# Optimization experiments

Measured on AMD Instinct MI355X. Metric: run time of the kernel, lower is better.

Reference implementation:

```python
import jax, jax.numpy as jnp
import numpy as np

WS = 8          # window_size
SHIFT = 4       # shift_size
NUM_HEADS = 8
DIM = 256
HIDDEN = 1024   # mlp_ratio * dim
EPS = 1e-5


def _rel_pos_index(ws):
    # static numpy computation of Swin relative position index, shape (ws*ws, ws*ws)
    coords = np.stack(np.meshgrid(np.arange(ws), np.arange(ws), indexing='ij')).reshape(2, -1)
    rel = coords[:, :, None] - coords[:, None, :]            # (2, N, N)
    rel = rel.transpose(1, 2, 0).astype(np.int64)            # (N, N, 2)
    rel[..., 0] += ws - 1
    rel[..., 1] += ws - 1
    rel[..., 0] *= 2 * ws - 1
    return rel.sum(-1)                                       # (N, N)

_REL_IDX = _rel_pos_index(WS)


def _layer_norm(x, g, b):
    m = jnp.mean(x, axis=-1, keepdims=True)
    v = jnp.mean(jnp.square(x - m), axis=-1, keepdims=True)
    return (x - m) * jax.lax.rsqrt(v + EPS) * g + b


def _window_partition(x, ws):
    B, H, W, C = x.shape
    x = x.reshape(B, H // ws, ws, W // ws, ws, C)
    return x.transpose(0, 1, 3, 2, 4, 5).reshape(-1, ws * ws, C)


def _window_reverse(win, ws, B, H, W):
    C = win.shape[-1]
    x = win.reshape(B, H // ws, W // ws, ws, ws, C)
    return x.transpose(0, 1, 3, 2, 4, 5).reshape(B, H, W, C)


def setup_inputs() -> dict:
    key = jax.random.key(0)
    ks = jax.random.split(key, 16)
    s = 0.02
    inp = {
        'x': jax.random.normal(ks[0], (8, 16384, 256), jnp.float32),
        'norm1_w': jnp.ones((DIM,), jnp.float32),
        'norm1_b': jnp.zeros((DIM,), jnp.float32),
        'qkv_w': jax.random.normal(ks[1], (3 * DIM, DIM), jnp.float32) * s,
        'qkv_b': jnp.zeros((3 * DIM,), jnp.float32),
        'rpb_table': jax.random.normal(ks[2], ((2 * WS - 1) * (2 * WS - 1), NUM_HEADS), jnp.float32) * s,
        'proj_w': jax.random.normal(ks[3], (DIM, DIM), jnp.float32) * s,
        'proj_b': jnp.zeros((DIM,), jnp.float32),
        'norm2_w': jnp.ones((DIM,), jnp.float32),
        'norm2_b': jnp.zeros((DIM,), jnp.float32),
        'fc1_w': jax.random.normal(ks[4], (HIDDEN, DIM), jnp.float32) * s,
        'fc1_b': jnp.zeros((HIDDEN,), jnp.float32),
        'fc2_w': jax.random.normal(ks[5], (DIM, HIDDEN), jnp.float32) * s,
        'fc2_b': jnp.zeros((DIM,), jnp.float32),
        'h': 128,
        'w': 128,
    }
    return inp


def reference(x, norm1_w, norm1_b, qkv_w, qkv_b, rpb_table, proj_w, proj_b,
              norm2_w, norm2_b, fc1_w, fc1_b, fc2_w, fc2_b, h, w):
    B, L, C = x.shape
    H, W = int(h), int(w)
    nh, hd = NUM_HEADS, C // NUM_HEADS
    scale = hd ** -0.5
    N = WS * WS

    shortcut = x
    xn = _layer_norm(x, norm1_w, norm1_b).reshape(B, H, W, C)
    # cyclic shift (SW-MSA)
    xs = jnp.roll(xn, shift=(-SHIFT, -SHIFT), axis=(1, 2))
    xw = _window_partition(xs, WS)                           # (B_, N, C)

    # window attention
    qkv = xw @ qkv_w.T + qkv_b                               # (B_, N, 3C)
    qkv = qkv.reshape(-1, N, 3, nh, hd).transpose(2, 0, 3, 1, 4)
    q, k, v = qkv[0], qkv[1], qkv[2]                         # (B_, nh, N, hd)
    attn = jnp.einsum('bhnd,bhmd->bhnm', q * scale, k)
    bias = rpb_table[_REL_IDX.reshape(-1)].reshape(N, N, nh).transpose(2, 0, 1)
    attn = jax.nn.softmax(attn + bias[None], axis=-1)
    out = jnp.einsum('bhnm,bhmd->bhnd', attn, v)
    out = out.transpose(0, 2, 1, 3).reshape(-1, N, C)
    out = out @ proj_w.T + proj_b

    # merge windows and reverse shift
    xs = _window_reverse(out, WS, B, H, W)
    xo = jnp.roll(xs, shift=(SHIFT, SHIFT), axis=(1, 2)).reshape(B, H * W, C)

    x = shortcut + xo
    # MLP with residual
    y = _layer_norm(x, norm2_w, norm2_b)
    y = jax.nn.gelu(y @ fc1_w.T + fc1_b, approximate=False)
    y = y @ fc2_w.T + fc2_b
    return x + y
```

## Files before the change

kernel.cpp:

```cpp
#include <hip/hip_runtime.h>

typedef __bf16 bf16_t;
typedef __bf16 bf16x4 __attribute__((ext_vector_type(4)));
typedef __bf16 bf16x8 __attribute__((ext_vector_type(8)));
typedef float f32x4 __attribute__((ext_vector_type(4)));

#define QKV_SEG 33554432L

#define GLDS(gp, lp)                                                                   \
  __builtin_amdgcn_global_load_lds((const __attribute__((address_space(1))) void*)(gp), \
                                   (__attribute__((address_space(3))) void*)(lp), 16, 0, 0)
#define BAR __builtin_amdgcn_s_barrier()
#define SCHED0 __builtin_amdgcn_sched_barrier(0)
#define MFMA __builtin_amdgcn_mfma_f32_16x16x32_bf16

__device__ inline float gelu_f(float u) {
  float c2 = 1.5957691216057308f * (u + 0.044715f * u * u * u);
  return u - u / (__expf(c2) + 1.0f);
}

__global__ __launch_bounds__(256) void cvt_kernel(const float* __restrict__ src,
                                                  bf16_t* __restrict__ dst) {
  int i = (blockIdx.x * 256 + threadIdx.x) * 4;
  float4 v = *(const float4*)(src + i);
  bf16x4 o;
  o[0] = (bf16_t)v.x; o[1] = (bf16_t)v.y; o[2] = (bf16_t)v.z; o[3] = (bf16_t)v.w;
  *(bf16x4*)(dst + i) = o;
}

__global__ __launch_bounds__(256) void ln_kernel(const float* __restrict__ src,
                                                 const float* __restrict__ gw,
                                                 const float* __restrict__ gb,
                                                 bf16_t* __restrict__ dst) {
  int lane = threadIdx.x & 63, wv = threadIdx.x >> 6;
  long m = (long)blockIdx.x * 4 + wv;
  long b_ = m >> 6; int tok = (int)(m & 63);
  int bb = (int)(b_ >> 8), win = (int)(b_ & 255);
  int wh = win >> 4, ww = win & 15;
  int ii = tok >> 3, jj = tok & 7;
  int hh = (wh * 8 + ii + 4) & 127, wp = (ww * 8 + jj + 4) & 127;
  long srow = ((long)bb << 14) + (hh << 7) + wp;

  float4 v = *(const float4*)(src + srow * 256 + lane * 4);
  float s = v.x + v.y + v.z + v.w;
  float s2 = v.x * v.x + v.y * v.y + v.z * v.z + v.w * v.w;
#pragma unroll
  for (int msk = 1; msk < 64; msk <<= 1) {
    s += __shfl_xor(s, msk);
    s2 += __shfl_xor(s2, msk);
  }
  float mean = s * (1.f / 256.f);
  float var = s2 * (1.f / 256.f) - mean * mean;
  float rs = rsqrtf(var + 1e-5f);
  float4 g4 = *(const float4*)(gw + lane * 4);
  float4 b4 = *(const float4*)(gb + lane * 4);
  bf16x4 o;
  o[0] = (bf16_t)((v.x - mean) * rs * g4.x + b4.x);
  o[1] = (bf16_t)((v.y - mean) * rs * g4.y + b4.y);
  o[2] = (bf16_t)((v.z - mean) * rs * g4.z + b4.z);
  o[3] = (bf16_t)((v.w - mean) * rs * g4.w + b4.w);
  *(bf16x4*)(dst + m * 256 + lane * 4) = o;
}

template <int EPI>
__global__ __launch_bounds__(256) void gemm_kernel(const bf16_t* __restrict__ A,
                                                   const bf16_t* __restrict__ Bw,
                                                   const float* __restrict__ bias, int K,
                                                   bf16_t* __restrict__ out_bf,
                                                   const float* resid) {
  __shared__ __align__(16) bf16_t As[2][8192];
  __shared__ __align__(16) bf16_t Bs[2][8192];
  int tid = threadIdx.x;
  int lane = tid & 63, wv = tid >> 6;
  int wm = wv >> 1, wn = wv & 1;

  int GX = gridDim.x, GY = gridDim.y;
  int flat = blockIdx.x + blockIdx.y * GX;
  int xcd = flat & 7, ii = flat >> 3;
  int iq = ii / GX;
  int by = xcd * (GY >> 3) + iq;
  int bx = ii - iq * GX;
  long m0 = (long)by * 128;
  int n0 = bx * 128;
  int lr = lane & 15, g = lane >> 4;

  int csw = (((lane & 7) ^ (lane >> 3)) << 3);
  const bf16_t* gA = A + (m0 + wv * 32 + (lane >> 3)) * K + csw;
  const bf16_t* gB = Bw + (long)(n0 + wv * 32 + (lane >> 3)) * K + csw;

  f32x4 acc[4][4] = {};

#define STAGE(buf, k0)                                                    \
  do {                                                                    \
    _Pragma("unroll") for (int s = 0; s < 4; ++s) {                       \
      GLDS(gA + (long)s * 8 * K + (k0), As[buf] + wv * 2048 + s * 512);   \
      GLDS(gB + (long)s * 8 * K + (k0), Bs[buf] + wv * 2048 + s * 512);   \
    }                                                                     \
  } while (0)

  int nt = K >> 6;
  STAGE(0, 0);
  for (int t = 0; t < nt; ++t) {
    int tb = t & 1;
    if (t + 1 < nt) {
      STAGE(tb ^ 1, (t + 1) << 6);
      asm volatile("s_waitcnt vmcnt(8)" ::: "memory");
    } else {
      asm volatile("s_waitcnt vmcnt(0)" ::: "memory");
    }
    BAR;
    SCHED0;
#pragma unroll
    for (int kk = 0; kk < 2; ++kk) {
      bf16x8 af[4], bfr[4];
#pragma unroll
      for (int mf = 0; mf < 4; ++mf)
        af[mf] = *(const bf16x8*)(As[tb] + (wm * 64 + mf * 16 + lr) * 64 +
                                  (((kk * 4 + g) ^ (lr & 7)) << 3));
#pragma unroll
      for (int nf = 0; nf < 4; ++nf)
        bfr[nf] = *(const bf16x8*)(Bs[tb] + (wn * 64 + nf * 16 + lr) * 64 +
                                   (((kk * 4 + g) ^ (lr & 7)) << 3));
#pragma unroll
      for (int mf = 0; mf < 4; ++mf)
#pragma unroll
        for (int nf = 0; nf < 4; ++nf)
          acc[mf][nf] = MFMA(af[mf], bfr[nf], acc[mf][nf], 0, 0, 0);
    }
    BAR;
  }
#undef STAGE

#pragma unroll
  for (int mf = 0; mf < 4; ++mf) {
#pragma unroll
    for (int nf = 0; nf < 4; ++nf) {
      long mb = m0 + wm * 64 + mf * 16 + 4 * g;
      int n = n0 + wn * 64 + nf * 16 + lr;
      float bn = bias[n];
      if (EPI == 0) {
        long b_ = mb >> 6;
        int tok = (int)(mb & 63);
        int which = n >> 8, rem = n & 255, head = rem >> 5, d = rem & 31;
        if (which == 2) {
          bf16x4 o;
#pragma unroll
          for (int r = 0; r < 4; ++r) o[r] = (bf16_t)(acc[mf][nf][r] + bn);
          *(bf16x4*)(out_bf + 2 * QKV_SEG + ((b_ * 8 + head) * 32 + d) * 64 + tok) = o;
        } else {
          long base = (long)which * QKV_SEG + ((b_ * 8 + head) * 64 + tok) * 32 + d;
#pragma unroll
          for (int r = 0; r < 4; ++r) out_bf[base + r * 32] = (bf16_t)(acc[mf][nf][r] + bn);
        }
      } else {
#pragma unroll
        for (int r = 0; r < 4; ++r) {
          long m = mb + r;
          long b_ = m >> 6; int tok = (int)(m & 63);
          int bb = (int)(b_ >> 8), win = (int)(b_ & 255);
          int wh = win >> 4, ww = win & 15;
          int jj0 = tok >> 3, jj = tok & 7;
          int hh = (wh * 8 + jj0 + 4) & 127, wp = (ww * 8 + jj + 4) & 127;
          long dst = (((long)bb << 14) + (hh << 7) + wp) * 256 + n;
          out_bf[dst] = (bf16_t)(acc[mf][nf][r] + bn + resid[dst]);
        }
      }
    }
  }
}

__global__ __launch_bounds__(512, 6) void mlp_kernel(const bf16_t* __restrict__ x1b,
                                                     float* __restrict__ out,
                                                     const float* __restrict__ gw,
                                                     const float* __restrict__ gb,
                                                     const bf16_t* __restrict__ w1,
                                                     const float* __restrict__ b1,
                                                     const bf16_t* __restrict__ w2,
                                                     const float* __restrict__ b2) {
  __shared__ __align__(16) bf16_t ys[64][264];
  __shared__ __align__(16) bf16_t hs[64][136];
  int tid = threadIdx.x, lane = tid & 63, wv = tid >> 6;
  long m0 = (long)blockIdx.x * 64;
  int lr = lane & 15, lk = (lane >> 4) * 8, g = lane >> 4;

  float4 g4 = *(const float4*)(gw + lane * 4);
  float4 b4 = *(const float4*)(gb + lane * 4);
#pragma unroll
  for (int i = 0; i < 8; ++i) {
    int r = wv * 8 + i;
    bf16x4 xv = *(const bf16x4*)(x1b + (m0 + r) * 256 + lane * 4);
    float v0 = (float)xv[0], v1 = (float)xv[1], v2 = (float)xv[2], v3 = (float)xv[3];
    float s = v0 + v1 + v2 + v3;
    float s2 = v0 * v0 + v1 * v1 + v2 * v2 + v3 * v3;
#pragma unroll
    for (int msk = 1; msk < 64; msk <<= 1) {
      s += __shfl_xor(s, msk);
      s2 += __shfl_xor(s2, msk);
    }
    float mean = s * (1.f / 256.f);
    float var = s2 * (1.f / 256.f) - mean * mean;
    float rs = rsqrtf(var + 1e-5f);
    bf16x4 o;
    o[0] = (bf16_t)((v0 - mean) * rs * g4.x + b4.x);
    o[1] = (bf16_t)((v1 - mean) * rs * g4.y + b4.y);
    o[2] = (bf16_t)((v2 - mean) * rs * g4.z + b4.z);
    o[3] = (bf16_t)((v3 - mean) * rs * g4.w + b4.w);
    *(bf16x4*)(&ys[r][lane * 4]) = o;
  }
  __syncthreads();

  f32x4 acc2[4][2] = {};

  for (int hc = 0; hc < 8; ++hc) {
    f32x4 acc1[4] = {};
#pragma unroll
    for (int half = 0; half < 2; ++half) {
      bf16x8 xf[4];
#pragma unroll
      for (int kb = 0; kb < 4; ++kb)
        xf[kb] = *(const bf16x8*)(w1 + (long)(hc * 128 + wv * 16 + lr) * 256 +
                                  (half * 4 + kb) * 32 + lk);
#pragma unroll
      for (int kb = 0; kb < 4; ++kb) {
        bf16x8 yf[4];
#pragma unroll
        for (int nt = 0; nt < 4; ++nt)
          yf[nt] = *(const bf16x8*)(&ys[nt * 16 + lr][(half * 4 + kb) * 32 + lk]);
#pragma unroll
        for (int nt = 0; nt < 4; ++nt) acc1[nt] = MFMA(xf[kb], yf[nt], acc1[nt], 0, 0, 0);
      }
    }
    {
      float4 bb = *(const float4*)(b1 + hc * 128 + wv * 16 + 4 * g);
#pragma unroll
      for (int nt = 0; nt < 4; ++nt) {
        bf16x4 o;
#pragma unroll
        for (int r = 0; r < 4; ++r) o[r] = (bf16_t)gelu_f(acc1[nt][r] + ((const float*)&bb)[r]);
        *(bf16x4*)(&hs[nt * 16 + lr][wv * 16 + 4 * g]) = o;
      }
    }
    __syncthreads();
#pragma unroll
    for (int half = 0; half < 2; ++half) {
      bf16x8 bw[2][2];
#pragma unroll
      for (int kb = 0; kb < 2; ++kb)
#pragma unroll
        for (int nf = 0; nf < 2; ++nf)
          bw[kb][nf] = *(const bf16x8*)(w2 + (long)(wv * 32 + nf * 16 + lr) * 1024 + hc * 128 +
                                        (half * 2 + kb) * 32 + lk);
#pragma unroll
      for (int kb = 0; kb < 2; ++kb) {
        bf16x8 ah[4];
#pragma unroll
        for (int mf = 0; mf < 4; ++mf)
          ah[mf] = *(const bf16x8*)(&hs[mf * 16 + lr][(half * 2 + kb) * 32 + lk]);
#pragma unroll
        for (int mf = 0; mf < 4; ++mf)
#pragma unroll
          for (int nf = 0; nf < 2; ++nf)
            acc2[mf][nf] = MFMA(ah[mf], bw[kb][nf], acc2[mf][nf], 0, 0, 0);
      }
    }
    __syncthreads();
  }

#pragma unroll
  for (int mf = 0; mf < 4; ++mf)
#pragma unroll
    for (int nf = 0; nf < 2; ++nf) {
      int n = wv * 32 + nf * 16 + lr;
      float bn = b2[n];
#pragma unroll
      for (int r = 0; r < 4; ++r) {
        long row = m0 + mf * 16 + 4 * g + r;
        out[row * 256 + n] = acc2[mf][nf][r] + bn + (float)x1b[row * 256 + n];
      }
    }
}

__global__ __launch_bounds__(256) void attn_kernel(const bf16_t* __restrict__ qkv,
                                                   const float* __restrict__ rpb,
                                                   bf16_t* __restrict__ attn_out) {
  __shared__ float rpb_s[1800];
  __shared__ bf16_t P[4][64][72];
  int tid = threadIdx.x, lane = tid & 63, wv = tid >> 6;
  long b_ = blockIdx.x;
  for (int i = tid; i < 1800; i += 256) rpb_s[i] = rpb[i];
  __syncthreads();
  const bf16_t* q = qkv;
  const bf16_t* k = qkv + QKV_SEG;
  const bf16_t* vt = qkv + 2 * QKV_SEG;
  int lr = lane & 15, lk = (lane >> 4) * 8, g = lane >> 4;
  const float scale = 0.17677669529663688f;

  for (int hh = 0; hh < 2; ++hh) {
    int head = wv * 2 + hh;
    long base = (b_ * 8 + head) * 2048;
    bf16x8 af[4], bfr[4];
#pragma unroll
    for (int mf = 0; mf < 4; ++mf)
      af[mf] = *(const bf16x8*)(q + base + (mf * 16 + lr) * 32 + lk);
#pragma unroll
    for (int nf = 0; nf < 4; ++nf)
      bfr[nf] = *(const bf16x8*)(k + base + (nf * 16 + lr) * 32 + lk);
    f32x4 S[4][4] = {};
#pragma unroll
    for (int mf = 0; mf < 4; ++mf)
#pragma unroll
      for (int nf = 0; nf < 4; ++nf)
        S[mf][nf] = MFMA(af[mf], bfr[nf], S[mf][nf], 0, 0, 0);
#pragma unroll
    for (int mf = 0; mf < 4; ++mf)
#pragma unroll
      for (int nf = 0; nf < 4; ++nf)
#pragma unroll
        for (int r = 0; r < 4; ++r) {
          int i = mf * 16 + 4 * g + r, j = nf * 16 + lr;
          int rel = ((i >> 3) - (j >> 3) + 7) * 15 + ((i & 7) - (j & 7) + 7);
          S[mf][nf][r] = S[mf][nf][r] * scale + rpb_s[rel * 8 + head];
        }
#pragma unroll
    for (int mf = 0; mf < 4; ++mf) {
#pragma unroll
      for (int r = 0; r < 4; ++r) {
        float mx = fmaxf(fmaxf(S[mf][0][r], S[mf][1][r]), fmaxf(S[mf][2][r], S[mf][3][r]));
#pragma unroll
        for (int msk = 1; msk < 16; msk <<= 1) mx = fmaxf(mx, __shfl_xor(mx, msk));
        float sm = 0.f;
#pragma unroll
        for (int nf = 0; nf < 4; ++nf) {
          float e = __expf(S[mf][nf][r] - mx);
          S[mf][nf][r] = e;
          sm += e;
        }
#pragma unroll
        for (int msk = 1; msk < 16; msk <<= 1) sm += __shfl_xor(sm, msk);
        float is = 1.f / sm;
        int i = mf * 16 + 4 * g + r;
#pragma unroll
        for (int nf = 0; nf < 4; ++nf) P[wv][i][nf * 16 + lr] = (bf16_t)(S[mf][nf][r] * is);
      }
    }
    f32x4 O[4][2] = {};
#pragma unroll
    for (int ks = 0; ks < 2; ++ks) {
      int j0 = ks * 32;
      bf16x8 pa[4], vb[2];
#pragma unroll
      for (int mf = 0; mf < 4; ++mf) pa[mf] = *(const bf16x8*)(&P[wv][mf * 16 + lr][j0 + lk]);
#pragma unroll
      for (int nf = 0; nf < 2; ++nf)
        vb[nf] = *(const bf16x8*)(vt + base + (nf * 16 + lr) * 64 + j0 + lk);
#pragma unroll
      for (int mf = 0; mf < 4; ++mf)
#pragma unroll
        for (int nf = 0; nf < 2; ++nf)
          O[mf][nf] = MFMA(pa[mf], vb[nf], O[mf][nf], 0, 0, 0);
    }
#pragma unroll
    for (int mf = 0; mf < 4; ++mf)
#pragma unroll
      for (int nf = 0; nf < 2; ++nf)
#pragma unroll
        for (int r = 0; r < 4; ++r) {
          int i = mf * 16 + 4 * g + r, d = nf * 16 + lr;
          attn_out[(b_ * 64 + i) * 256 + head * 32 + d] = (bf16_t)O[mf][nf][r];
        }
  }
}

extern "C" void kernel_launch(void* const* d_in, const int* in_sizes, int n_in,
                              void* d_out, int out_size, void* d_ws, size_t ws_size,
                              hipStream_t stream) {
  const float* x = (const float*)d_in[0];
  const float* n1w = (const float*)d_in[1];
  const float* n1b = (const float*)d_in[2];
  const float* qkv_w = (const float*)d_in[3];
  const float* qkv_b = (const float*)d_in[4];
  const float* rpb = (const float*)d_in[5];
  const float* proj_w = (const float*)d_in[6];
  const float* proj_b = (const float*)d_in[7];
  const float* n2w = (const float*)d_in[8];
  const float* n2b = (const float*)d_in[9];
  const float* fc1_w = (const float*)d_in[10];
  const float* fc1_b = (const float*)d_in[11];
  const float* fc2_w = (const float*)d_in[12];
  const float* fc2_b = (const float*)d_in[13];
  float* out = (float*)d_out;

  char* ws = (char*)d_ws;
  bf16_t* bufA = (bf16_t*)ws;
  bf16_t* x1b = (bf16_t*)(ws + 201326592L);
  bf16_t* bufB = (bf16_t*)(ws + 268435456L);
  bf16_t* wq = (bf16_t*)(ws + 335544320L);
  bf16_t* wp = wq + 196608;
  bf16_t* w1 = wp + 65536;
  bf16_t* w2 = w1 + 262144;

  cvt_kernel<<<192, 256, 0, stream>>>(qkv_w, wq);
  cvt_kernel<<<64, 256, 0, stream>>>(proj_w, wp);
  cvt_kernel<<<256, 256, 0, stream>>>(fc1_w, w1);
  cvt_kernel<<<256, 256, 0, stream>>>(fc2_w, w2);

  ln_kernel<<<32768, 256, 0, stream>>>(x, n1w, n1b, bufB);
  gemm_kernel<0><<<dim3(6, 1024), 256, 0, stream>>>(bufB, wq, qkv_b, 256, bufA, nullptr);
  attn_kernel<<<2048, 256, 0, stream>>>(bufA, rpb, bufB);
  gemm_kernel<1><<<dim3(2, 1024), 256, 0, stream>>>(bufB, wp, proj_b, 256, x1b, x);
  mlp_kernel<<<2048, 512, 0, stream>>>(x1b, out, n2w, n2b, w1, fc1_b, w2, fc2_b);
}
```

Baseline: 602.4 us.

## Fuse output projection and residual into window attention kernel

```diff
diff --git a/kernel.cpp b/kernel.cpp
--- a/kernel.cpp
+++ b/kernel.cpp
@@ -62,12 +62,10 @@
   *(bf16x4*)(dst + m * 256 + lane * 4) = o;
 }
 
-template <int EPI>
 __global__ __launch_bounds__(256) void gemm_kernel(const bf16_t* __restrict__ A,
                                                    const bf16_t* __restrict__ Bw,
                                                    const float* __restrict__ bias, int K,
-                                                   bf16_t* __restrict__ out_bf,
-                                                   const float* resid) {
+                                                   bf16_t* __restrict__ out_bf) {
   __shared__ __align__(16) bf16_t As[2][8192];
   __shared__ __align__(16) bf16_t Bs[2][8192];
   int tid = threadIdx.x;
@@ -138,34 +136,160 @@
       long mb = m0 + wm * 64 + mf * 16 + 4 * g;
       int n = n0 + wn * 64 + nf * 16 + lr;
       float bn = bias[n];
-      if (EPI == 0) {
-        long b_ = mb >> 6;
-        int tok = (int)(mb & 63);
-        int which = n >> 8, rem = n & 255, head = rem >> 5, d = rem & 31;
-        if (which == 2) {
-          bf16x4 o;
-#pragma unroll
-          for (int r = 0; r < 4; ++r) o[r] = (bf16_t)(acc[mf][nf][r] + bn);
-          *(bf16x4*)(out_bf + 2 * QKV_SEG + ((b_ * 8 + head) * 32 + d) * 64 + tok) = o;
-        } else {
-          long base = (long)which * QKV_SEG + ((b_ * 8 + head) * 64 + tok) * 32 + d;
-#pragma unroll
-          for (int r = 0; r < 4; ++r) out_bf[base + r * 32] = (bf16_t)(acc[mf][nf][r] + bn);
+      long b_ = mb >> 6;
+      int tok = (int)(mb & 63);
+      int which = n >> 8, rem = n & 255, head = rem >> 5, d = rem & 31;
+      if (which == 2) {
+        bf16x4 o;
+#pragma unroll
+        for (int r = 0; r < 4; ++r) o[r] = (bf16_t)(acc[mf][nf][r] + bn);
+        *(bf16x4*)(out_bf + 2 * QKV_SEG + ((b_ * 8 + head) * 32 + d) * 64 + tok) = o;
+      } else {
+        long base = (long)which * QKV_SEG + ((b_ * 8 + head) * 64 + tok) * 32 + d;
+#pragma unroll
+        for (int r = 0; r < 4; ++r) out_bf[base + r * 32] = (bf16_t)(acc[mf][nf][r] + bn);
+      }
+    }
+  }
+}
+
+__global__ __launch_bounds__(256) void attn2_kernel(const bf16_t* __restrict__ qkv,
+                                                    const float* __restrict__ rpb,
+                                                    const bf16_t* __restrict__ wp,
+                                                    const float* __restrict__ proj_b,
+                                                    const float* __restrict__ x,
+                                                    bf16_t* __restrict__ x1b) {
+  __shared__ float rpb_s[1800];
+  __shared__ bf16_t P[4][64][72];
+  __shared__ bf16_t ao[64][264];
+  int tid = threadIdx.x, lane = tid & 63, wv = tid >> 6;
+  long b_ = blockIdx.x;
+  for (int i = tid; i < 1800; i += 256) rpb_s[i] = rpb[i];
+  __syncthreads();
+  const bf16_t* q = qkv;
+  const bf16_t* k = qkv + QKV_SEG;
+  const bf16_t* vt = qkv + 2 * QKV_SEG;
+  int lr = lane & 15, lk = (lane >> 4) * 8, g = lane >> 4;
+  const float scale = 0.17677669529663688f;
+
+  for (int hh = 0; hh < 2; ++hh) {
+    int head = wv * 2 + hh;
+    long base = (b_ * 8 + head) * 2048;
+    bf16x8 af[4], bfr[4];
+#pragma unroll
+    for (int mf = 0; mf < 4; ++mf)
+      af[mf] = *(const bf16x8*)(q + base + (mf * 16 + lr) * 32 + lk);
+#pragma unroll
+    for (int nf = 0; nf < 4; ++nf)
+      bfr[nf] = *(const bf16x8*)(k + base + (nf * 16 + lr) * 32 + lk);
+    f32x4 S[4][4] = {};
+#pragma unroll
+    for (int mf = 0; mf < 4; ++mf)
+#pragma unroll
+      for (int nf = 0; nf < 4; ++nf)
+        S[mf][nf] = MFMA(af[mf], bfr[nf], S[mf][nf], 0, 0, 0);
+#pragma unroll
+    for (int mf = 0; mf < 4; ++mf)
+#pragma unroll
+      for (int nf = 0; nf < 4; ++nf)
+#pragma unroll
+        for (int r = 0; r < 4; ++r) {
+          int i = mf * 16 + 4 * g + r, j = nf * 16 + lr;
+          int rel = ((i >> 3) - (j >> 3) + 7) * 15 + ((i & 7) - (j & 7) + 7);
+          S[mf][nf][r] = S[mf][nf][r] * scale + rpb_s[rel * 8 + head];
         }
-      } else {
+#pragma unroll
+    for (int mf = 0; mf < 4; ++mf) {
+#pragma unroll
+      for (int r = 0; r < 4; ++r) {
+        float mx = fmaxf(fmaxf(S[mf][0][r], S[mf][1][r]), fmaxf(S[mf][2][r], S[mf][3][r]));
+#pragma unroll
+        for (int msk = 1; msk < 16; msk <<= 1) mx = fmaxf(mx, __shfl_xor(mx, msk));
+        float sm = 0.f;
+#pragma unroll
+        for (int nf = 0; nf < 4; ++nf) {
+          float e = __expf(S[mf][nf][r] - mx);
+          S[mf][nf][r] = e;
+          sm += e;
+        }
+#pragma unroll
+        for (int msk = 1; msk < 16; msk <<= 1) sm += __shfl_xor(sm, msk);
+        float is = 1.f / sm;
+        int i = mf * 16 + 4 * g + r;
+#pragma unroll
+        for (int nf = 0; nf < 4; ++nf) P[wv][i][nf * 16 + lr] = (bf16_t)(S[mf][nf][r] * is);
+      }
+    }
+    f32x4 O[4][2] = {};
+#pragma unroll
+    for (int ks = 0; ks < 2; ++ks) {
+      int j0 = ks * 32;
+      bf16x8 pa[4], vb[2];
+#pragma unroll
+      for (int mf = 0; mf < 4; ++mf) pa[mf] = *(const bf16x8*)(&P[wv][mf * 16 + lr][j0 + lk]);
+#pragma unroll
+      for (int nf = 0; nf < 2; ++nf)
+        vb[nf] = *(const bf16x8*)(vt + base + (nf * 16 + lr) * 64 + j0 + lk);
+#pragma unroll
+      for (int mf = 0; mf < 4; ++mf)
+#pragma unroll
+        for (int nf = 0; nf < 2; ++nf)
+          O[mf][nf] = MFMA(pa[mf], vb[nf], O[mf][nf], 0, 0, 0);
+    }
+#pragma unroll
+    for (int mf = 0; mf < 4; ++mf)
+#pragma unroll
+      for (int nf = 0; nf < 2; ++nf)
 #pragma unroll
         for (int r = 0; r < 4; ++r) {
-          long m = mb + r;
-          long b_ = m >> 6; int tok = (int)(m & 63);
-          int bb = (int)(b_ >> 8), win = (int)(b_ & 255);
-          int wh = win >> 4, ww = win & 15;
-          int jj0 = tok >> 3, jj = tok & 7;
-          int hh = (wh * 8 + jj0 + 4) & 127, wp = (ww * 8 + jj + 4) & 127;
-          long dst = (((long)bb << 14) + (hh << 7) + wp) * 256 + n;
-          out_bf[dst] = (bf16_t)(acc[mf][nf][r] + bn + resid[dst]);
+          int i = mf * 16 + 4 * g + r, d = nf * 16 + lr;
+          ao[i][head * 32 + d] = (bf16_t)O[mf][nf][r];
         }
-      }
-    }
+  }
+  __syncthreads();
+
+  f32x4 pacc[4][4] = {};
+#pragma unroll
+  for (int half = 0; half < 4; ++half) {
+    bf16x8 bw[2][4];
+#pragma unroll
+    for (int kb = 0; kb < 2; ++kb)
+#pragma unroll
+      for (int nf = 0; nf < 4; ++nf)
+        bw[kb][nf] = *(const bf16x8*)(wp + (long)(wv * 64 + nf * 16 + lr) * 256 +
+                                      (half * 2 + kb) * 32 + lk);
+#pragma unroll
+    for (int kb = 0; kb < 2; ++kb) {
+      bf16x8 paf[4];
+#pragma unroll
+      for (int mf = 0; mf < 4; ++mf)
+        paf[mf] = *(const bf16x8*)(&ao[mf * 16 + lr][(half * 2 + kb) * 32 + lk]);
+#pragma unroll
+      for (int mf = 0; mf < 4; ++mf)
+#pragma unroll
+        for (int nf = 0; nf < 4; ++nf)
+          pacc[mf][nf] = MFMA(paf[mf], bw[kb][nf], pacc[mf][nf], 0, 0, 0);
+    }
+  }
+
+  {
+    int bb = (int)(b_ >> 8), win = (int)(b_ & 255);
+    int wh = win >> 4, ww = win & 15;
+#pragma unroll
+    for (int mf = 0; mf < 4; ++mf)
+#pragma unroll
+      for (int nf = 0; nf < 4; ++nf) {
+        int n = wv * 64 + nf * 16 + lr;
+        float bn = proj_b[n];
+#pragma unroll
+        for (int r = 0; r < 4; ++r) {
+          int tok = mf * 16 + 4 * g + r;
+          int ii = tok >> 3, jj = tok & 7;
+          int hh = (wh * 8 + ii + 4) & 127, wpp = (ww * 8 + jj + 4) & 127;
+          long dst = (((long)bb << 14) + (hh << 7) + wpp) * 256 + n;
+          x1b[dst] = (bf16_t)(pacc[mf][nf][r] + bn + x[dst]);
+        }
+      }
   }
 }
 
@@ -278,97 +402,6 @@
         out[row * 256 + n] = acc2[mf][nf][r] + bn + (float)x1b[row * 256 + n];
       }
     }
-}
-
-__global__ __launch_bounds__(256) void attn_kernel(const bf16_t* __restrict__ qkv,
-                                                   const float* __restrict__ rpb,
-                                                   bf16_t* __restrict__ attn_out) {
-  __shared__ float rpb_s[1800];
-  __shared__ bf16_t P[4][64][72];
-  int tid = threadIdx.x, lane = tid & 63, wv = tid >> 6;
-  long b_ = blockIdx.x;
-  for (int i = tid; i < 1800; i += 256) rpb_s[i] = rpb[i];
-  __syncthreads();
-  const bf16_t* q = qkv;
-  const bf16_t* k = qkv + QKV_SEG;
-  const bf16_t* vt = qkv + 2 * QKV_SEG;
-  int lr = lane & 15, lk = (lane >> 4) * 8, g = lane >> 4;
-  const float scale = 0.17677669529663688f;
-
-  for (int hh = 0; hh < 2; ++hh) {
-    int head = wv * 2 + hh;
-    long base = (b_ * 8 + head) * 2048;
-    bf16x8 af[4], bfr[4];
-#pragma unroll
-    for (int mf = 0; mf < 4; ++mf)
-      af[mf] = *(const bf16x8*)(q + base + (mf * 16 + lr) * 32 + lk);
-#pragma unroll
-    for (int nf = 0; nf < 4; ++nf)
-      bfr[nf] = *(const bf16x8*)(k + base + (nf * 16 + lr) * 32 + lk);
-    f32x4 S[4][4] = {};
-#pragma unroll
-    for (int mf = 0; mf < 4; ++mf)
-#pragma unroll
-      for (int nf = 0; nf < 4; ++nf)
-        S[mf][nf] = MFMA(af[mf], bfr[nf], S[mf][nf], 0, 0, 0);
-#pragma unroll
-    for (int mf = 0; mf < 4; ++mf)
-#pragma unroll
-      for (int nf = 0; nf < 4; ++nf)
-#pragma unroll
-        for (int r = 0; r < 4; ++r) {
-          int i = mf * 16 + 4 * g + r, j = nf * 16 + lr;
-          int rel = ((i >> 3) - (j >> 3) + 7) * 15 + ((i & 7) - (j & 7) + 7);
-          S[mf][nf][r] = S[mf][nf][r] * scale + rpb_s[rel * 8 + head];
-        }
-#pragma unroll
-    for (int mf = 0; mf < 4; ++mf) {
-#pragma unroll
-      for (int r = 0; r < 4; ++r) {
-        float mx = fmaxf(fmaxf(S[mf][0][r], S[mf][1][r]), fmaxf(S[mf][2][r], S[mf][3][r]));
-#pragma unroll
-        for (int msk = 1; msk < 16; msk <<= 1) mx = fmaxf(mx, __shfl_xor(mx, msk));
-        float sm = 0.f;
-#pragma unroll
-        for (int nf = 0; nf < 4; ++nf) {
-          float e = __expf(S[mf][nf][r] - mx);
-          S[mf][nf][r] = e;
-          sm += e;
-        }
-#pragma unroll
-        for (int msk = 1; msk < 16; msk <<= 1) sm += __shfl_xor(sm, msk);
-        float is = 1.f / sm;
-        int i = mf * 16 + 4 * g + r;
-#pragma unroll
-        for (int nf = 0; nf < 4; ++nf) P[wv][i][nf * 16 + lr] = (bf16_t)(S[mf][nf][r] * is);
-      }
-    }
-    f32x4 O[4][2] = {};
-#pragma unroll
-    for (int ks = 0; ks < 2; ++ks) {
-      int j0 = ks * 32;
-      bf16x8 pa[4], vb[2];
-#pragma unroll
-      for (int mf = 0; mf < 4; ++mf) pa[mf] = *(const bf16x8*)(&P[wv][mf * 16 + lr][j0 + lk]);
-#pragma unroll
-      for (int nf = 0; nf < 2; ++nf)
-        vb[nf] = *(const bf16x8*)(vt + base + (nf * 16 + lr) * 64 + j0 + lk);
-#pragma unroll
-      for (int mf = 0; mf < 4; ++mf)
-#pragma unroll
-        for (int nf = 0; nf < 2; ++nf)
-          O[mf][nf] = MFMA(pa[mf], vb[nf], O[mf][nf], 0, 0, 0);
-    }
-#pragma unroll
-    for (int mf = 0; mf < 4; ++mf)
-#pragma unroll
-      for (int nf = 0; nf < 2; ++nf)
-#pragma unroll
-        for (int r = 0; r < 4; ++r) {
-          int i = mf * 16 + 4 * g + r, d = nf * 16 + lr;
-          attn_out[(b_ * 64 + i) * 256 + head * 32 + d] = (bf16_t)O[mf][nf][r];
-        }
-  }
 }
 
 extern "C" void kernel_launch(void* const* d_in, const int* in_sizes, int n_in,
@@ -405,8 +438,7 @@
   cvt_kernel<<<256, 256, 0, stream>>>(fc2_w, w2);
 
   ln_kernel<<<32768, 256, 0, stream>>>(x, n1w, n1b, bufB);
-  gemm_kernel<0><<<dim3(6, 1024), 256, 0, stream>>>(bufB, wq, qkv_b, 256, bufA, nullptr);
-  attn_kernel<<<2048, 256, 0, stream>>>(bufA, rpb, bufB);
-  gemm_kernel<1><<<dim3(2, 1024), 256, 0, stream>>>(bufB, wp, proj_b, 256, x1b, x);
+  gemm_kernel<<<dim3(6, 1024), 256, 0, stream>>>(bufB, wq, qkv_b, 256, bufA);
+  attn2_kernel<<<2048, 256, 0, stream>>>(bufA, rpb, wp, proj_b, x, x1b);
   mlp_kernel<<<2048, 512, 0, stream>>>(x1b, out, n2w, n2b, w1, fc1_b, w2, fc2_b);
 }
```

Result: slower. 685.4 us (+13.8%).
